# Kernel optimization log

Measured on AMD Instinct MI355X. Metric: run time of the kernel, lower is better.

Reference implementation:

```python
import jax, jax.numpy as jnp
import numpy as np

N, T, F = 128, 512, 3
H = 5          # hidden_channels
NEURONS = 2000


def setup_inputs() -> dict:
    key = jax.random.key(0)
    ks = jax.random.split(key, 8)
    s = 0.3  # keep exp() outputs in a sane range
    return {
        "x": jax.random.normal(ks[0], (N, T, F), dtype=jnp.float32),
        "w_ih": jax.random.normal(ks[1], (3 * H, F), dtype=jnp.float32) * s,
        "w_hh": jax.random.normal(ks[2], (3 * H, H), dtype=jnp.float32) * s,
        "b_ih": jax.random.normal(ks[3], (3 * H,), dtype=jnp.float32) * s,
        "b_hh": jax.random.normal(ks[4], (3 * H,), dtype=jnp.float32) * s,
        "lw": jax.random.normal(ks[5], (NEURONS, H), dtype=jnp.float32) * s,
        "lb": jax.random.normal(ks[6], (NEURONS,), dtype=jnp.float32) * s,
    }


def _gru_states(x, w_ih, w_hh, b_ih, b_hh):
    # x: [N, T, F] -> hidden states [T, N, H] via lax.scan (PyTorch GRUCell math)
    n_batch = x.shape[0]
    h0 = jnp.zeros((n_batch, w_hh.shape[1]), dtype=x.dtype)

    def step(h, xt):
        gi = xt @ w_ih.T + b_ih              # [N, 3H]
        gh = h @ w_hh.T + b_hh               # [N, 3H]
        i_r, i_z, i_n = jnp.split(gi, 3, axis=1)
        h_r, h_z, h_n = jnp.split(gh, 3, axis=1)
        r = jax.nn.sigmoid(i_r + h_r)
        z = jax.nn.sigmoid(i_z + h_z)
        n = jnp.tanh(i_n + r * h_n)
        h_new = (1.0 - z) * n + z * h
        return h_new, h_new

    _, hs = jax.lax.scan(step, h0, jnp.swapaxes(x, 0, 1))
    return hs  # [T, N, H]


def reference(x, w_ih, w_hh, b_ih, b_hh, lw, lb):
    hs = _gru_states(x, w_ih, w_hh, b_ih, b_hh)          # [T, N, H]
    states = jnp.swapaxes(hs, 0, 1)                      # [N, T, H] (== stack(states, 1))
    out = jnp.exp(jnp.einsum("nth,oh->nto", states, lw) + lb)  # [N, T, NEURONS]
    return out
```

## Files before the change

kernel.cpp:

```cpp
#include <hip/hip_runtime.h>
#include <hip/hip_bf16.h>

#define N_BATCH 128
#define T_STEPS 512
#define F_IN 3
#define H_DIM 5
#define NEURONS 2000
#define NT (N_BATCH * T_STEPS)

__device__ __forceinline__ float fast_rcp(float x) {
    return __builtin_amdgcn_rcpf(x);
}

__device__ __forceinline__ float fast_sigmoid(float x) {
    return fast_rcp(1.0f + __expf(-x));
}

__device__ __forceinline__ float fast_tanh(float x) {
    float t = __expf(x + x);
    return (t - 1.0f) * fast_rcp(t + 1.0f);
}

__global__ __launch_bounds__(64, 1) void gru_kernel(
    const float* __restrict__ x,
    const float* __restrict__ w_ih,
    const float* __restrict__ w_hh,
    const float* __restrict__ b_ih,
    const float* __restrict__ b_hh,
    float* __restrict__ states)
{
    const int gid = blockIdx.x * 64 + threadIdx.x;
    const int n = gid >> 3;
    const int j = threadIdx.x & 7;
    const int jj = (j < 5) ? j : 4;

    float wir[F_IN], wiz[F_IN], win[F_IN];
    float whr[H_DIM], whz[H_DIM], whn[H_DIM];
#pragma unroll
    for (int f = 0; f < F_IN; ++f) {
        wir[f] = w_ih[(jj)          * F_IN + f];
        wiz[f] = w_ih[(H_DIM + jj)  * F_IN + f];
        win[f] = w_ih[(2*H_DIM + jj)* F_IN + f];
    }
#pragma unroll
    for (int i = 0; i < H_DIM; ++i) {
        whr[i] = w_hh[(jj)          * H_DIM + i];
        whz[i] = w_hh[(H_DIM + jj)  * H_DIM + i];
        whn[i] = w_hh[(2*H_DIM + jj)* H_DIM + i];
    }
    const float br  = b_ih[jj]           + b_hh[jj];
    const float bz  = b_ih[H_DIM + jj]   + b_hh[H_DIM + jj];
    const float bin = b_ih[2*H_DIM + jj];
    const float bhn = b_hh[2*H_DIM + jj];

    float h = 0.0f;

    const float* xp = x + (size_t)n * T_STEPS * F_IN;
    float* sp = states + (size_t)n * T_STEPS * H_DIM;

    for (int t = 0; t < T_STEPS; ++t) {
        const float x0 = xp[t * F_IN + 0];
        const float x1 = xp[t * F_IN + 1];
        const float x2 = xp[t * F_IN + 2];

        const float h0 = __shfl(h, 0, 8);
        const float h1 = __shfl(h, 1, 8);
        const float h2 = __shfl(h, 2, 8);
        const float h3 = __shfl(h, 3, 8);
        const float h4 = __shfl(h, 4, 8);

        float ar = br + x0*wir[0] + x1*wir[1] + x2*wir[2]
                      + h0*whr[0] + h1*whr[1] + h2*whr[2] + h3*whr[3] + h4*whr[4];
        float az = bz + x0*wiz[0] + x1*wiz[1] + x2*wiz[2]
                      + h0*whz[0] + h1*whz[1] + h2*whz[2] + h3*whz[3] + h4*whz[4];
        float gin = bin + x0*win[0] + x1*win[1] + x2*win[2];
        float ghn = bhn + h0*whn[0] + h1*whn[1] + h2*whn[2] + h3*whn[3] + h4*whn[4];

        const float r  = fast_sigmoid(ar);
        const float z  = fast_sigmoid(az);
        const float nn = fast_tanh(gin + r * ghn);
        h = (1.0f - z) * nn + z * h;

        if (j < 5) sp[t * H_DIM + j] = h;
    }
}

__global__ __launch_bounds__(256) void readout_kernel(
    const float* __restrict__ states,
    const float* __restrict__ lw,
    const float* __restrict__ lb,
    float* __restrict__ out)
{
    const int tid = threadIdx.x;
    const bool active = (tid * 8) < NEURONS;
    const int o0 = tid * 8;

    float w[8][H_DIM];
    float b[8];
    if (active) {
#pragma unroll
        for (int i = 0; i < 8; ++i) {
            b[i] = lb[o0 + i];
#pragma unroll
            for (int jj = 0; jj < H_DIM; ++jj) w[i][jj] = lw[(o0 + i) * H_DIM + jj];
        }
    }

    for (int p = blockIdx.x; p < NT; p += gridDim.x) {
        const float* hp = states + (size_t)p * H_DIM;
        const float h0 = hp[0], h1 = hp[1], h2 = hp[2], h3 = hp[3], h4 = hp[4];
        if (active) {
            float v[8];
#pragma unroll
            for (int i = 0; i < 8; ++i) {
                float a = b[i] + w[i][0] * h0 + w[i][1] * h1 + w[i][2] * h2 +
                          w[i][3] * h3 + w[i][4] * h4;
                v[i] = __expf(a);
            }
            float4* op = (float4*)(out + (size_t)p * NEURONS + o0);
            op[0] = make_float4(v[0], v[1], v[2], v[3]);
            op[1] = make_float4(v[4], v[5], v[6], v[7]);
        }
    }
}

extern "C" void kernel_launch(void* const* d_in, const int* in_sizes, int n_in,
                              void* d_out, int out_size, void* d_ws, size_t ws_size,
                              hipStream_t stream) {
    const float* x    = (const float*)d_in[0];
    const float* w_ih = (const float*)d_in[1];
    const float* w_hh = (const float*)d_in[2];
    const float* b_ih = (const float*)d_in[3];
    const float* b_hh = (const float*)d_in[4];
    const float* lw   = (const float*)d_in[5];
    const float* lb   = (const float*)d_in[6];
    float* out = (float*)d_out;

    float* states = (float*)d_ws;

    gru_kernel<<<16, 64, 0, stream>>>(x, w_ih, w_hh, b_ih, b_hh, states);
    readout_kernel<<<2048, 256, 0, stream>>>(states, lw, lb, out);
}
```

Baseline: 672.4 us.

## Stage GRU inputs in LDS, pad state rows, coalesce readout stores

```diff
diff --git a/kernel.cpp b/kernel.cpp
--- a/kernel.cpp
+++ b/kernel.cpp
@@ -7,6 +7,8 @@
 #define H_DIM 5
 #define NEURONS 2000
 #define NT (N_BATCH * T_STEPS)
+#define SROW 8
+#define XLDS_STRIDE 1540
 
 __device__ __forceinline__ float fast_rcp(float x) {
     return __builtin_amdgcn_rcpf(x);
@@ -29,39 +31,56 @@
     const float* __restrict__ b_hh,
     float* __restrict__ states)
 {
-    const int gid = blockIdx.x * 64 + threadIdx.x;
-    const int n = gid >> 3;
-    const int j = threadIdx.x & 7;
+    __shared__ float xs[8 * XLDS_STRIDE];
+
+    const int tid = threadIdx.x;
+    const int b   = blockIdx.x;
+
+    const float* xg = x + (size_t)b * 8 * T_STEPS * F_IN;
+    for (int e4 = tid; e4 < (8 * T_STEPS * F_IN) / 4; e4 += 64) {
+        float4 v = ((const float4*)xg)[e4];
+        int e   = e4 * 4;
+        int nl  = e / (T_STEPS * F_IN);
+        int off = e - nl * (T_STEPS * F_IN);
+        float* d = &xs[nl * XLDS_STRIDE + off];
+        d[0] = v.x; d[1] = v.y; d[2] = v.z; d[3] = v.w;
+    }
+    __syncthreads();
+
+    const int nl = tid >> 3;
+    const int j  = tid & 7;
     const int jj = (j < 5) ? j : 4;
 
     float wir[F_IN], wiz[F_IN], win[F_IN];
     float whr[H_DIM], whz[H_DIM], whn[H_DIM];
 #pragma unroll
     for (int f = 0; f < F_IN; ++f) {
-        wir[f] = w_ih[(jj)          * F_IN + f];
-        wiz[f] = w_ih[(H_DIM + jj)  * F_IN + f];
-        win[f] = w_ih[(2*H_DIM + jj)* F_IN + f];
+        wir[f] = w_ih[(jj)            * F_IN + f];
+        wiz[f] = w_ih[(H_DIM + jj)    * F_IN + f];
+        win[f] = w_ih[(2*H_DIM + jj)  * F_IN + f];
     }
 #pragma unroll
     for (int i = 0; i < H_DIM; ++i) {
-        whr[i] = w_hh[(jj)          * H_DIM + i];
-        whz[i] = w_hh[(H_DIM + jj)  * H_DIM + i];
-        whn[i] = w_hh[(2*H_DIM + jj)* H_DIM + i];
+        whr[i] = w_hh[(jj)            * H_DIM + i];
+        whz[i] = w_hh[(H_DIM + jj)    * H_DIM + i];
+        whn[i] = w_hh[(2*H_DIM + jj)  * H_DIM + i];
     }
-    const float br  = b_ih[jj]           + b_hh[jj];
-    const float bz  = b_ih[H_DIM + jj]   + b_hh[H_DIM + jj];
+    const float br  = b_ih[jj]          + b_hh[jj];
+    const float bz  = b_ih[H_DIM + jj]  + b_hh[H_DIM + jj];
     const float bin = b_ih[2*H_DIM + jj];
     const float bhn = b_hh[2*H_DIM + jj];
 
+    const float* xl = &xs[nl * XLDS_STRIDE];
+    float* sp = states + (size_t)(b * 8 + nl) * T_STEPS * SROW;
+
     float h = 0.0f;
-
-    const float* xp = x + (size_t)n * T_STEPS * F_IN;
-    float* sp = states + (size_t)n * T_STEPS * H_DIM;
+    float nx0 = xl[0], nx1 = xl[1], nx2 = xl[2];
 
     for (int t = 0; t < T_STEPS; ++t) {
-        const float x0 = xp[t * F_IN + 0];
-        const float x1 = xp[t * F_IN + 1];
-        const float x2 = xp[t * F_IN + 2];
+        const float x0 = nx0, x1 = nx1, x2 = nx2;
+        nx0 = xl[(t + 1) * 3 + 0];
+        nx1 = xl[(t + 1) * 3 + 1];
+        nx2 = xl[(t + 1) * 3 + 2];
 
         const float h0 = __shfl(h, 0, 8);
         const float h1 = __shfl(h, 1, 8);
@@ -81,7 +100,7 @@
         const float nn = fast_tanh(gin + r * ghn);
         h = (1.0f - z) * nn + z * h;
 
-        if (j < 5) sp[t * H_DIM + j] = h;
+        sp[t * SROW + j] = h;
     }
 }
 
@@ -92,34 +111,48 @@
     float* __restrict__ out)
 {
     const int tid = threadIdx.x;
-    const bool active = (tid * 8) < NEURONS;
-    const int o0 = tid * 8;
+    const int o1 = tid * 4;
+    const int o2 = 1024 + tid * 4;
+    const bool act2 = o2 < NEURONS;
 
-    float w[8][H_DIM];
-    float b[8];
-    if (active) {
+    float w1[4][H_DIM], b1[4];
+    float w2[4][H_DIM], b2[4];
 #pragma unroll
-        for (int i = 0; i < 8; ++i) {
-            b[i] = lb[o0 + i];
+    for (int i = 0; i < 4; ++i) {
+        b1[i] = lb[o1 + i];
 #pragma unroll
-            for (int jj = 0; jj < H_DIM; ++jj) w[i][jj] = lw[(o0 + i) * H_DIM + jj];
+        for (int k = 0; k < H_DIM; ++k) w1[i][k] = lw[(o1 + i) * H_DIM + k];
+    }
+    if (act2) {
+#pragma unroll
+        for (int i = 0; i < 4; ++i) {
+            b2[i] = lb[o2 + i];
+#pragma unroll
+            for (int k = 0; k < H_DIM; ++k) w2[i][k] = lw[(o2 + i) * H_DIM + k];
         }
     }
 
     for (int p = blockIdx.x; p < NT; p += gridDim.x) {
-        const float* hp = states + (size_t)p * H_DIM;
-        const float h0 = hp[0], h1 = hp[1], h2 = hp[2], h3 = hp[3], h4 = hp[4];
-        if (active) {
-            float v[8];
-#pragma unroll
-            for (int i = 0; i < 8; ++i) {
-                float a = b[i] + w[i][0] * h0 + w[i][1] * h1 + w[i][2] * h2 +
-                          w[i][3] * h3 + w[i][4] * h4;
-                v[i] = __expf(a);
-            }
-            float4* op = (float4*)(out + (size_t)p * NEURONS + o0);
-            op[0] = make_float4(v[0], v[1], v[2], v[3]);
-            op[1] = make_float4(v[4], v[5], v[6], v[7]);
+        const float* hp = states + (size_t)p * SROW;
+        const float4 hv = *(const float4*)hp;
+        const float h4  = hp[4];
+
+        float* row = out + (size_t)p * NEURONS;
+
+        float4 v1;
+        v1.x = __expf(b1[0] + w1[0][0]*hv.x + w1[0][1]*hv.y + w1[0][2]*hv.z + w1[0][3]*hv.w + w1[0][4]*h4);
+        v1.y = __expf(b1[1] + w1[1][0]*hv.x + w1[1][1]*hv.y + w1[1][2]*hv.z + w1[1][3]*hv.w + w1[1][4]*h4);
+        v1.z = __expf(b1[2] + w1[2][0]*hv.x + w1[2][1]*hv.y + w1[2][2]*hv.z + w1[2][3]*hv.w + w1[2][4]*h4);
+        v1.w = __expf(b1[3] + w1[3][0]*hv.x + w1[3][1]*hv.y + w1[3][2]*hv.z + w1[3][3]*hv.w + w1[3][4]*h4);
+        ((float4*)row)[tid] = v1;
+
+        if (act2) {
+            float4 v2;
+            v2.x = __expf(b2[0] + w2[0][0]*hv.x + w2[0][1]*hv.y + w2[0][2]*hv.z + w2[0][3]*hv.w + w2[0][4]*h4);
+            v2.y = __expf(b2[1] + w2[1][0]*hv.x + w2[1][1]*hv.y + w2[1][2]*hv.z + w2[1][3]*hv.w + w2[1][4]*h4);
+            v2.z = __expf(b2[2] + w2[2][0]*hv.x + w2[2][1]*hv.y + w2[2][2]*hv.z + w2[2][3]*hv.w + w2[2][4]*h4);
+            v2.w = __expf(b2[3] + w2[3][0]*hv.x + w2[3][1]*hv.y + w2[3][2]*hv.z + w2[3][3]*hv.w + w2[3][4]*h4);
+            *(float4*)(row + o2) = v2;
         }
     }
 }
```

New measurement: 634.9 us. 1.06x faster.
